# Kernel optimization log

Hardware: AMD Instinct MI355X
Metric: run time of the kernel (lower is better)

The kernel has to match this reference:

```python
import jax, jax.numpy as jnp
import numpy as np

B, T, H, I = 128, 1024, 512, 64
DT, TAU, NOISE_VAR = 1.0, 10.0, 0.1


def setup_inputs() -> dict:
    key = jax.random.key(0)
    k1, k2, k3, k4 = jax.random.split(key, 4)
    x = jax.random.normal(k1, (B, T, I), dtype=jnp.float32)
    # W_in: rows have unit-ish norm in the original init; normal/sqrt(I) is equivalent scale
    W_in = jax.random.normal(k2, (H, I), dtype=jnp.float32) / np.float32(np.sqrt(I))
    # W_hidden: randn/sqrt(H) then spectral-radius normalized; /sqrt(H) gives radius ~1
    W_hidden = jax.random.normal(k3, (H, H), dtype=jnp.float32) / np.float32(np.sqrt(H))
    # noise drawn inside forward in the original; materialized here: N(0, noise_var)
    sigma = jax.random.normal(k4, (H, T, B), dtype=jnp.float32) * np.float32(NOISE_VAR)
    h0 = jnp.zeros((H, B), dtype=jnp.float32)
    return {"x": x, "W_in": W_in, "W_hidden": W_hidden, "sigma": sigma, "h0": h0}


def reference(x, W_in, W_hidden, sigma, h0):
    c1 = jnp.float32(1.0 - DT / TAU)
    c2 = jnp.float32(DT / TAU)
    # precomputed input projection: [T, H, B] (scan carries over leading T axis)
    w_input = jnp.einsum("hi,bti->thb", W_in, x)
    sig = jnp.transpose(sigma, (1, 0, 2))  # [T, H, B]

    def step(h, inp):
        w_in_t, s_t = inp
        w_h = W_hidden @ jax.nn.sigmoid(h)          # [H, B]
        h_new = c1 * h + c2 * (w_in_t + w_h + s_t)  # leaky integration
        return h_new, h_new.T                        # emit [B, H]

    h_last, out_tbh = jax.lax.scan(step, h0, (w_input, sig))
    out = jnp.transpose(out_tbh, (1, 0, 2))  # [B, T, H]
    return out, h_last
```

## Files before the change

kernel.cpp:

```cpp
#include <hip/hip_runtime.h>
#include <stdint.h>

#define B_  128
#define T_  1024
#define H_  512
#define I_  64
#define TB_ 131072

typedef _Float16 half2_t __attribute__((ext_vector_type(2)));

union U32H2 { uint32_t u; half2_t h; };
union U16H  { uint16_t u; _Float16 h; };

static __device__ __forceinline__ half2_t u2h(uint32_t u){ U32H2 x; x.u=u; return x.h; }
static __device__ __forceinline__ uint32_t h2u(half2_t h){ U32H2 x; x.h=h; return x.u; }

#if defined(__has_builtin)
#if __has_builtin(__builtin_amdgcn_fdot2)
#define HAVE_FDOT2 1
#endif
#endif

static __device__ __forceinline__ float fdot2f(half2_t a, half2_t b, float c){
#ifdef HAVE_FDOT2
    return __builtin_amdgcn_fdot2(a, b, c, false);
#else
    return c + (float)a[0]*(float)b[0] + (float)a[1]*(float)b[1];
#endif
}

__global__ __launch_bounds__(256) void k_wingemm(const float* __restrict__ x,
                                                 const float* __restrict__ Win,
                                                 uint32_t* __restrict__ r2)
{
    __shared__ float As[128*65];
    __shared__ float Ws[64*65];
    const int t   = blockIdx.x;
    const int j0  = blockIdx.y * 64;
    const int tid = threadIdx.x;

#pragma unroll
    for (int k = 0; k < 8; k++){
        int qid = k*256 + tid;
        int row = qid >> 4;
        int qq  = qid & 15;
        float4 v = *(const float4*)(x + ((size_t)row*T_ + t)*I_ + qq*4);
        float* d = As + row*65 + qq*4;
        d[0]=v.x; d[1]=v.y; d[2]=v.z; d[3]=v.w;
    }
#pragma unroll
    for (int k = 0; k < 4; k++){
        int qid = k*256 + tid;
        int row = qid >> 4;
        int qq  = qid & 15;
        float4 v = *(const float4*)(Win + (size_t)(j0+row)*I_ + qq*4);
        float* d = Ws + row*65 + qq*4;
        d[0]=v.x; d[1]=v.y; d[2]=v.z; d[3]=v.w;
    }
    __syncthreads();

    const int tj = tid & 15;
    const int tb = tid >> 4;

    float acc[8][2][2];
#pragma unroll
    for (int bb=0; bb<8; bb++)
#pragma unroll
        for (int jj=0; jj<2; jj++){ acc[bb][jj][0]=0.f; acc[bb][jj][1]=0.f; }

#pragma unroll 4
    for (int i = 0; i < 64; i++){
        float a[8];
#pragma unroll
        for (int bb=0; bb<8; bb++) a[bb] = As[(tb + 16*bb)*65 + i];
        float wv[2][2];
#pragma unroll
        for (int jj=0; jj<2; jj++){
            wv[jj][0] = Ws[(2*tj + 32*jj    )*65 + i];
            wv[jj][1] = Ws[(2*tj + 32*jj + 1)*65 + i];
        }
#pragma unroll
        for (int bb=0; bb<8; bb++)
#pragma unroll
            for (int jj=0; jj<2; jj++){
                acc[bb][jj][0] += a[bb]*wv[jj][0];
                acc[bb][jj][1] += a[bb]*wv[jj][1];
            }
    }

#pragma unroll
    for (int bb=0; bb<8; bb++){
        int mi = t*128 + tb + 16*bb;
#pragma unroll
        for (int jj=0; jj<2; jj++){
            half2_t hv; hv[0]=(_Float16)acc[bb][jj][0]; hv[1]=(_Float16)acc[bb][jj][1];
            r2[(size_t)mi*256 + (j0>>1) + tj + 16*jj] = h2u(hv);
        }
    }
}

static __device__ __forceinline__ uint32_t addpair(uint32_t u, float a0, float a1){
    half2_t h = u2h(u);
    half2_t o; o[0]=(_Float16)((float)h[0] + a0); o[1]=(_Float16)((float)h[1] + a1);
    return h2u(o);
}

__global__ __launch_bounds__(256) void k_addsig(const float* __restrict__ sigma,
                                                uint32_t* __restrict__ r2)
{
    __shared__ float Ss[64*256];
    const int mi0 = blockIdx.x * 256;
    const int j0  = blockIdx.y * 64;
    const int tid = threadIdx.x;

#pragma unroll
    for (int k = 0; k < 16; k++){
        int qid = k*256 + tid;
        int row = qid >> 6;
        int qq  = qid & 63;
        float4 v = *(const float4*)(sigma + (size_t)(j0+row)*TB_ + mi0 + qq*4);
        *(float4*)(Ss + row*256 + qq*4) = v;
    }
    __syncthreads();

    const int mi = mi0 + tid;
    uint32_t* rr = r2 + (size_t)mi*256 + (j0>>1);
#pragma unroll
    for (int k = 0; k < 8; k++){
        uint4 q = *(uint4*)(rr + 4*k);
        q.x = addpair(q.x, Ss[(8*k+0)*256+tid], Ss[(8*k+1)*256+tid]);
        q.y = addpair(q.y, Ss[(8*k+2)*256+tid], Ss[(8*k+3)*256+tid]);
        q.z = addpair(q.z, Ss[(8*k+4)*256+tid], Ss[(8*k+5)*256+tid]);
        q.w = addpair(q.w, Ss[(8*k+6)*256+tid], Ss[(8*k+7)*256+tid]);
        *(uint4*)(rr + 4*k) = q;
    }
}

__global__ __launch_bounds__(512, 2) void k_rnn(const float* __restrict__ Wh,
                                                const float* __restrict__ Win,
                                                const float* __restrict__ x,
                                                const float* __restrict__ sigma,
                                                const float* __restrict__ h0,
                                                const uint16_t* __restrict__ r16,
                                                float* __restrict__ out,
                                                int use_r)
{
    extern __shared__ char smem[];
    uint32_t*  WL  = (uint32_t*)smem;
    float*     par = (float*)(smem + 131072);
    _Float16*  sb  = (_Float16*)(smem + 147456);

    const int b = blockIdx.x;
    const int t = threadIdx.x;
    const int w = t >> 6;
    const int l = t & 63;
    const int j = t;
    const int phase = (l & 15) << 2;

    half2_t wreg[6][32];
#pragma unroll
    for (int m = 0; m < 8; m++){
        const int row = l + 64*m;
        const float4* wr = (const float4*)(Wh + (size_t)row*H_ + (w << 6));
#pragma unroll
        for (int q = 0; q < 16; q++){
            float4 v = wr[q];
            half2_t a; a[0]=(_Float16)v.x; a[1]=(_Float16)v.y;
            half2_t c; c[0]=(_Float16)v.z; c[1]=(_Float16)v.w;
            int pp = 2*q;
            if (m < 6){
                wreg[m][pp]   = a;
                wreg[m][pp+1] = c;
            } else {
                int base = (m-6)*32;
                WL[t*64 + ((base + pp     + phase) & 63)] = h2u(a);
                WL[t*64 + ((base + pp + 1 + phase) & 63)] = h2u(c);
            }
        }
    }

    float h = h0[(size_t)j*B_ + b];
    const uint32_t* WLt = WL + t*64;
    const uint32_t* sbu = (const uint32_t*)sb;
    float* outp = out + (size_t)b*T_*H_ + j;
    const uint16_t* rp = r16 + (size_t)b*H_ + j;

    for (int ts = 0; ts < T_; ts++){
        uint16_t ru = 0;
        if (use_r) ru = rp[(size_t)ts * 65536];

        float e = __expf(-h);
        float s = 1.0f / (1.0f + e);
        sb[j] = (_Float16)s;
        __syncthreads();

        float p[8];
#pragma unroll
        for (int m = 0; m < 8; m++) p[m] = 0.f;

#pragma unroll
        for (int c = 0; c < 8; c++){
            uint4 sq = *(const uint4*)(sbu + (w << 5) + (c << 2));
            half2_t s0=u2h(sq.x), s1=u2h(sq.y), s2=u2h(sq.z), s3=u2h(sq.w);
            uint4 q6 = *(const uint4*)(WLt + ((4*c      + phase) & 63));
            uint4 q7 = *(const uint4*)(WLt + ((32 + 4*c + phase) & 63));
#pragma unroll
            for (int m = 0; m < 6; m++){
                p[m] = fdot2f(wreg[m][4*c+0], s0, p[m]);
                p[m] = fdot2f(wreg[m][4*c+1], s1, p[m]);
                p[m] = fdot2f(wreg[m][4*c+2], s2, p[m]);
                p[m] = fdot2f(wreg[m][4*c+3], s3, p[m]);
            }
            p[6] = fdot2f(u2h(q6.x), s0, p[6]);
            p[6] = fdot2f(u2h(q6.y), s1, p[6]);
            p[6] = fdot2f(u2h(q6.z), s2, p[6]);
            p[6] = fdot2f(u2h(q6.w), s3, p[6]);
            p[7] = fdot2f(u2h(q7.x), s0, p[7]);
            p[7] = fdot2f(u2h(q7.y), s1, p[7]);
            p[7] = fdot2f(u2h(q7.z), s2, p[7]);
            p[7] = fdot2f(u2h(q7.w), s3, p[7]);
        }

#pragma unroll
        for (int m = 0; m < 8; m++) par[(w << 9) + l + (m << 6)] = p[m];
        __syncthreads();

        float P = par[j] + par[j+512] + par[j+1024] + par[j+1536]
                + par[j+2048] + par[j+2560] + par[j+3072] + par[j+3584];

        float rv;
        if (use_r){
            U16H cv; cv.u = ru;
            rv = (float)cv.h;
        } else {
            float acc = 0.f;
            const float4* wir = (const float4*)(Win + (size_t)j*I_);
            const float4* xr  = (const float4*)(x + ((size_t)b*T_ + ts)*I_);
#pragma unroll
            for (int q = 0; q < 16; q++){
                float4 a = wir[q]; float4 xx = xr[q];
                acc += a.x*xx.x + a.y*xx.y + a.z*xx.z + a.w*xx.w;
            }
            rv = acc + sigma[((size_t)j << 17) + (ts << 7) + b];
        }

        h = 0.9f*h + 0.1f*(P + rv);
        outp[(size_t)ts * H_] = h;
    }

    out[(size_t)B_*T_*H_ + (size_t)j*B_ + b] = h;
}

extern "C" void kernel_launch(void* const* d_in, const int* in_sizes, int n_in,
                              void* d_out, int out_size, void* d_ws, size_t ws_size,
                              hipStream_t stream)
{
    const float* x     = (const float*)d_in[0];
    const float* Win   = (const float*)d_in[1];
    const float* Wh    = (const float*)d_in[2];
    const float* sigma = (const float*)d_in[3];
    const float* h0    = (const float*)d_in[4];
    float* out = (float*)d_out;

    const size_t r_bytes = (size_t)TB_ * H_ * 2;
    const int use_r = (ws_size >= r_bytes) ? 1 : 0;

    if (use_r){
        k_wingemm<<<dim3(T_, 8), 256, 0, stream>>>(x, Win, (uint32_t*)d_ws);
        k_addsig <<<dim3(TB_/256, 8), 256, 0, stream>>>(sigma, (uint32_t*)d_ws);
    }

    const int lds_bytes = 131072 + 16384 + 1024;
    (void)hipFuncSetAttribute((const void*)k_rnn,
                              hipFuncAttributeMaxDynamicSharedMemorySize, lds_bytes);
    k_rnn<<<B_, 512, lds_bytes, stream>>>(Wh, Win, x, sigma, h0,
                                          (const uint16_t*)d_ws, out, use_r);
}
```

Before: 2.516 ms.

## Fuse sigma add into input GEMM, use lighter barriers and padded partial-sum layout

```diff
diff --git a/kernel.cpp b/kernel.cpp
--- a/kernel.cpp
+++ b/kernel.cpp
@@ -29,8 +29,15 @@
 #endif
 }
 
+#define BARRIER_NODRAIN() do {                                        \
+    __asm__ __volatile__("s_waitcnt lgkmcnt(0)" ::: "memory");        \
+    __builtin_amdgcn_s_barrier();                                     \
+    __asm__ __volatile__("" ::: "memory");                            \
+} while (0)
+
 __global__ __launch_bounds__(256) void k_wingemm(const float* __restrict__ x,
                                                  const float* __restrict__ Win,
+                                                 const float* __restrict__ sigma,
                                                  uint32_t* __restrict__ r2)
 {
     __shared__ float As[128*65];
@@ -87,52 +94,32 @@
                 acc[bb][jj][1] += a[bb]*wv[jj][1];
             }
     }
+    __syncthreads();
+
+    float* Sg = As;
+#pragma unroll
+    for (int k = 0; k < 8; k++){
+        int qid = k*256 + tid;
+        int row = qid >> 5;
+        int qq  = qid & 31;
+        float4 v = *(const float4*)(sigma + (size_t)(j0+row)*TB_ + (size_t)t*128 + qq*4);
+        float* d = Sg + row*130 + qq*4;
+        d[0]=v.x; d[1]=v.y; d[2]=v.z; d[3]=v.w;
+    }
+    __syncthreads();
 
 #pragma unroll
     for (int bb=0; bb<8; bb++){
-        int mi = t*128 + tb + 16*bb;
+        int bcol = tb + 16*bb;
+        int mi = t*128 + bcol;
 #pragma unroll
         for (int jj=0; jj<2; jj++){
-            half2_t hv; hv[0]=(_Float16)acc[bb][jj][0]; hv[1]=(_Float16)acc[bb][jj][1];
+            int jA = 2*tj + 32*jj;
+            float a0 = acc[bb][jj][0] + Sg[(jA    )*130 + bcol];
+            float a1 = acc[bb][jj][1] + Sg[(jA + 1)*130 + bcol];
+            half2_t hv; hv[0]=(_Float16)a0; hv[1]=(_Float16)a1;
             r2[(size_t)mi*256 + (j0>>1) + tj + 16*jj] = h2u(hv);
         }
-    }
-}
-
-static __device__ __forceinline__ uint32_t addpair(uint32_t u, float a0, float a1){
-    half2_t h = u2h(u);
-    half2_t o; o[0]=(_Float16)((float)h[0] + a0); o[1]=(_Float16)((float)h[1] + a1);
-    return h2u(o);
-}
-
-__global__ __launch_bounds__(256) void k_addsig(const float* __restrict__ sigma,
-                                                uint32_t* __restrict__ r2)
-{
-    __shared__ float Ss[64*256];
-    const int mi0 = blockIdx.x * 256;
-    const int j0  = blockIdx.y * 64;
-    const int tid = threadIdx.x;
-
-#pragma unroll
-    for (int k = 0; k < 16; k++){
-        int qid = k*256 + tid;
-        int row = qid >> 6;
-        int qq  = qid & 63;
-        float4 v = *(const float4*)(sigma + (size_t)(j0+row)*TB_ + mi0 + qq*4);
-        *(float4*)(Ss + row*256 + qq*4) = v;
-    }
-    __syncthreads();
-
-    const int mi = mi0 + tid;
-    uint32_t* rr = r2 + (size_t)mi*256 + (j0>>1);
-#pragma unroll
-    for (int k = 0; k < 8; k++){
-        uint4 q = *(uint4*)(rr + 4*k);
-        q.x = addpair(q.x, Ss[(8*k+0)*256+tid], Ss[(8*k+1)*256+tid]);
-        q.y = addpair(q.y, Ss[(8*k+2)*256+tid], Ss[(8*k+3)*256+tid]);
-        q.z = addpair(q.z, Ss[(8*k+4)*256+tid], Ss[(8*k+5)*256+tid]);
-        q.w = addpair(q.w, Ss[(8*k+6)*256+tid], Ss[(8*k+7)*256+tid]);
-        *(uint4*)(rr + 4*k) = q;
     }
 }
 
@@ -148,7 +135,7 @@
     extern __shared__ char smem[];
     uint32_t*  WL  = (uint32_t*)smem;
     float*     par = (float*)(smem + 131072);
-    _Float16*  sb  = (_Float16*)(smem + 147456);
+    _Float16*  sb  = (_Float16*)(smem + 131072 + 18432);
 
     const int b = blockIdx.x;
     const int t = threadIdx.x;
@@ -192,7 +179,7 @@
         float e = __expf(-h);
         float s = 1.0f / (1.0f + e);
         sb[j] = (_Float16)s;
-        __syncthreads();
+        BARRIER_NODRAIN();
 
         float p[8];
 #pragma unroll
@@ -222,11 +209,12 @@
         }
 
 #pragma unroll
-        for (int m = 0; m < 8; m++) par[(w << 9) + l + (m << 6)] = p[m];
-        __syncthreads();
-
-        float P = par[j] + par[j+512] + par[j+1024] + par[j+1536]
-                + par[j+2048] + par[j+2560] + par[j+3072] + par[j+3584];
+        for (int m = 0; m < 8; m++) par[(l + (m << 6))*9 + w] = p[m];
+        BARRIER_NODRAIN();
+
+        const float* pj = par + j*9;
+        float P = ((pj[0] + pj[1]) + (pj[2] + pj[3]))
+                + ((pj[4] + pj[5]) + (pj[6] + pj[7]));
 
         float rv;
         if (use_r){
@@ -266,11 +254,10 @@
     const int use_r = (ws_size >= r_bytes) ? 1 : 0;
 
     if (use_r){
-        k_wingemm<<<dim3(T_, 8), 256, 0, stream>>>(x, Win, (uint32_t*)d_ws);
-        k_addsig <<<dim3(TB_/256, 8), 256, 0, stream>>>(sigma, (uint32_t*)d_ws);
-    }
-
-    const int lds_bytes = 131072 + 16384 + 1024;
+        k_wingemm<<<dim3(T_, 8), 256, 0, stream>>>(x, Win, sigma, (uint32_t*)d_ws);
+    }
+
+    const int lds_bytes = 131072 + 18432 + 1024;
     (void)hipFuncSetAttribute((const void*)k_rnn,
                               hipFuncAttributeMaxDynamicSharedMemorySize, lds_bytes);
     k_rnn<<<B_, 512, lds_bytes, stream>>>(Wh, Win, x, sigma, h0,
```

After: 2.375 ms. 1.06x faster.
